# Kernel tuning notes

Measured on AMD Instinct MI355X. Metric: run time of the kernel, lower is better.

Reference implementation:

```python
import jax, jax.numpy as jnp
import numpy as np

D_MODEL = 768
D_STATE = 16
D_CONV = 4
EXPAND = 2
D_INNER = EXPAND * D_MODEL
DT_RANK = (D_MODEL + 15) // 16  # 48
BATCH = 2
SEQ = 1024
LN_EPS = 1e-5


def setup_inputs() -> dict:
    key = jax.random.key(0)
    ks = jax.random.split(key, 12)
    s = 0.02
    inp = {
        "x": jax.random.normal(ks[0], (BATCH, SEQ, D_MODEL), dtype=jnp.float32),
        "in_proj_w": jax.random.normal(ks[1], (2 * D_INNER, D_MODEL), dtype=jnp.float32) * s,
        "conv_w": jax.random.normal(ks[2], (D_INNER, D_CONV), dtype=jnp.float32) * s,
        "conv_b": jnp.zeros((D_INNER,), dtype=jnp.float32),
        "x_proj_w": jax.random.normal(ks[3], (DT_RANK + 2 * D_STATE, D_INNER), dtype=jnp.float32) * s,
        "dt_proj_w": jax.random.normal(ks[4], (D_INNER, DT_RANK), dtype=jnp.float32) * s,
        "dt_proj_b": jnp.full((D_INNER,), -4.0, dtype=jnp.float32),  # softplus(-4) ~ small dt
        "A_log": jnp.log(jnp.broadcast_to(jnp.arange(1, D_STATE + 1, dtype=jnp.float32), (D_INNER, D_STATE))),
        "D": jnp.ones((D_INNER,), dtype=jnp.float32),
        "out_proj_w": jax.random.normal(ks[5], (D_MODEL, D_INNER), dtype=jnp.float32) * s,
        "ln_w": jnp.ones((D_MODEL,), dtype=jnp.float32),
        "ln_b": jnp.zeros((D_MODEL,), dtype=jnp.float32),
    }
    return inp


def _mamba(x, in_proj_w, conv_w, conv_b, x_proj_w, dt_proj_w, dt_proj_b, A_log, D, out_proj_w):
    B, L, _ = x.shape
    # input projection -> [B, L, 2*D_INNER], split into x-branch and gate z
    xz = jnp.einsum("bld,ed->ble", x, in_proj_w)
    xb, z = jnp.split(xz, 2, axis=-1)
    # causal depthwise conv1d along L
    lhs = jnp.transpose(xb, (0, 2, 1))  # [B, D_INNER, L]
    rhs = conv_w[:, None, :]  # [D_INNER, 1, D_CONV]
    xc = jax.lax.conv_general_dilated(
        lhs, rhs, window_strides=(1,), padding=[(D_CONV - 1, 0)],
        dimension_numbers=("NCH", "OIH", "NCH"), feature_group_count=D_INNER)
    xc = jnp.transpose(xc, (0, 2, 1)) + conv_b  # [B, L, D_INNER]
    xc = jax.nn.silu(xc)
    # data-dependent SSM parameters
    x_dbl = jnp.einsum("bld,ed->ble", xc, x_proj_w)  # [B, L, DT_RANK+2*D_STATE]
    dt, Bm, Cm = jnp.split(x_dbl, [DT_RANK, DT_RANK + D_STATE], axis=-1)
    dt = jax.nn.softplus(jnp.einsum("blr,dr->bld", dt, dt_proj_w) + dt_proj_b)  # [B, L, D_INNER]
    A = -jnp.exp(A_log)  # [D_INNER, D_STATE]

    # selective scan over time
    def step(h, inp):
        dt_t, B_t, C_t, u_t = inp  # [B,D_INNER], [B,D_STATE], [B,D_STATE], [B,D_INNER]
        dA = jnp.exp(dt_t[:, :, None] * A)  # [B, D_INNER, D_STATE]
        h = h * dA + (dt_t * u_t)[:, :, None] * B_t[:, None, :]
        y = jnp.einsum("bds,bs->bd", h, C_t)
        return h, y

    h0 = jnp.zeros((B, D_INNER, D_STATE), dtype=x.dtype)
    xs = (jnp.transpose(dt, (1, 0, 2)), jnp.transpose(Bm, (1, 0, 2)),
          jnp.transpose(Cm, (1, 0, 2)), jnp.transpose(xc, (1, 0, 2)))
    _, ys = jax.lax.scan(step, h0, xs)  # ys: [L, B, D_INNER]
    y = jnp.transpose(ys, (1, 0, 2)) + xc * D
    y = y * jax.nn.silu(z)
    return jnp.einsum("ble,de->bld", y, out_proj_w)  # [B, L, D_MODEL]


def reference(x, in_proj_w, conv_w, conv_b, x_proj_w, dt_proj_w, dt_proj_b,
              A_log, D, out_proj_w, ln_w, ln_b):
    residual = x
    h = _mamba(x, in_proj_w, conv_w, conv_b, x_proj_w, dt_proj_w, dt_proj_b, A_log, D, out_proj_w)
    # dropout is identity in eval mode
    y = h + residual
    mu = jnp.mean(y, axis=-1, keepdims=True)
    var = jnp.mean(jnp.square(y - mu), axis=-1, keepdims=True)
    return (y - mu) * jax.lax.rsqrt(var + LN_EPS) * ln_w + ln_b
```

## Files before the change

kernel.cpp:

```cpp
#include <hip/hip_runtime.h>
#include <hip/hip_bf16.h>
#include <math.h>

#define BATCH   2
#define SEQ     1024
#define DMODEL  768
#define DINNER  1536
#define DSTATE  16
#define DTRANK  48
#define NTOK    (BATCH*SEQ)
#define XPROJ_N (DTRANK + 2*DSTATE)
#define XP_PSZ  ((size_t)NTOK * XPROJ_N)

#define LC      32
#define NC      (SEQ/LC)

#define KSPL_IN   2
#define KSPL_OUT  4
#define KSPL_XP   8

typedef unsigned short ushort_t;
typedef __attribute__((ext_vector_type(8))) short bf16x8;
typedef __attribute__((ext_vector_type(4))) float f32x4;

__device__ __forceinline__ ushort_t f2bf(float f) {
    unsigned int u = __float_as_uint(f);
    u += 0x7FFF + ((u >> 16) & 1);
    return (ushort_t)(u >> 16);
}

__global__ __launch_bounds__(256)
void f2b_3(const float* __restrict__ s0, ushort_t* __restrict__ d0, int n0,
           const float* __restrict__ s1, ushort_t* __restrict__ d1, int n1,
           const float* __restrict__ s2, ushort_t* __restrict__ d2, int n2)
{
    const int i = (blockIdx.x * 256 + threadIdx.x) * 4;
    const float* s; ushort_t* d;
    if (i < n0)               { s = s0 + i;            d = d0 + i; }
    else if (i < n0 + n1)     { s = s1 + (i - n0);     d = d1 + (i - n0); }
    else if (i < n0 + n1 + n2){ s = s2 + (i - n0 - n1);d = d2 + (i - n0 - n1); }
    else return;
    const float4 v = *reinterpret_cast<const float4*>(s);
    ushort4 o;
    o.x = f2bf(v.x); o.y = f2bf(v.y); o.z = f2bf(v.z); o.w = f2bf(v.w);
    *reinterpret_cast<ushort4*>(d) = o;
}

#define GLOAD_LDS16(gp, lp) \
    __builtin_amdgcn_global_load_lds((const __attribute__((address_space(1))) void*)(gp), \
                                     (__attribute__((address_space(3))) void*)(lp), 16, 0, 0)

__global__ __launch_bounds__(256)
void gemm_mfma_bt_sk(const ushort_t* __restrict__ A, const ushort_t* __restrict__ W,
                     float* __restrict__ C, int M, int N, int K, int klen)
{
    __shared__ ushort_t As[128 * 32];
    __shared__ ushort_t Bs[128 * 32];

    const int tid  = threadIdx.x;
    const int w    = tid >> 6;
    const int lane = tid & 63;
    const int m0 = blockIdx.y * 128;
    const int n0 = blockIdx.x * 128;
    const int kbeg = blockIdx.z * klen;
    float* Cp = C + (size_t)blockIdx.z * M * N;

    const int lrow = lane >> 2;
    const int lcol = (lane & 3) * 8;

    const ushort_t* ga0 = A + (size_t)(m0 + w * 16 + lrow) * K + kbeg + lcol;
    const ushort_t* ga1 = ga0 + (size_t)64 * K;
    const ushort_t* gb0 = W + (size_t)(n0 + w * 16 + lrow) * K + kbeg + lcol;
    const ushort_t* gb1 = gb0 + (size_t)64 * K;

    ushort_t* lA0 = As + w * 512;
    ushort_t* lA1 = As + 64 * 32 + w * 512;
    ushort_t* lB0 = Bs + w * 512;
    ushort_t* lB1 = Bs + 64 * 32 + w * 512;

    const int wm = w >> 1, wn = w & 1;
    const int fr = lane & 15;
    const int kg = lane >> 4;

    f32x4 acc[4][4] = {};

    for (int kt = 0; kt < klen; kt += 32) {
        __syncthreads();
        GLOAD_LDS16(ga0 + kt, lA0);
        GLOAD_LDS16(ga1 + kt, lA1);
        GLOAD_LDS16(gb0 + kt, lB0);
        GLOAD_LDS16(gb1 + kt, lB1);
        __syncthreads();

        bf16x8 af[4], bfr[4];
        #pragma unroll
        for (int i = 0; i < 4; ++i) {
            af[i]  = *reinterpret_cast<const bf16x8*>(&As[(wm * 64 + i * 16 + fr) * 32 + kg * 8]);
            bfr[i] = *reinterpret_cast<const bf16x8*>(&Bs[(wn * 64 + i * 16 + fr) * 32 + kg * 8]);
        }
        #pragma unroll
        for (int i = 0; i < 4; ++i)
            #pragma unroll
            for (int j = 0; j < 4; ++j)
                acc[i][j] = __builtin_amdgcn_mfma_f32_16x16x32_bf16(af[i], bfr[j], acc[i][j], 0, 0, 0);
    }

    #pragma unroll
    for (int i = 0; i < 4; ++i) {
        const int row_base = m0 + wm * 64 + i * 16 + kg * 4;
        #pragma unroll
        for (int j = 0; j < 4; ++j) {
            const int col = n0 + wn * 64 + j * 16 + fr;
            #pragma unroll
            for (int r = 0; r < 4; ++r)
                Cp[(size_t)(row_base + r) * N + col] = acc[i][j][r];
        }
    }
}

#define BM 64
#define BN 64
#define BK 16

__global__ __launch_bounds__(256)
void gemm_tn_xp(const float* __restrict__ A, const float* __restrict__ W,
                float* __restrict__ C)
{
    __shared__ float As[BK][BM + 4];
    __shared__ float Ws[BK][BN + 4];

    const int M = NTOK, N = XPROJ_N, K = DINNER, lda = DINNER;
    const int kchunk = DINNER / KSPL_XP;

    const int t  = threadIdx.x;
    const int tx = t & 15;
    const int ty = t >> 4;
    const int row0 = blockIdx.y * BM;
    const int col0 = blockIdx.x * BN;
    const int kbeg = blockIdx.z * kchunk;
    const int kend = kbeg + kchunk;
    float* Cp = C + (size_t)blockIdx.z * XP_PSZ;

    const int m_l = t >> 2;
    const int k_l = (t & 3) * 4;

    float acc[4][4] = {};

    for (int kt = kbeg; kt < kend; kt += BK) {
        float4 av, wv;
        {
            const float* ap = A + (size_t)(row0 + m_l) * lda + kt + k_l;
            av = *reinterpret_cast<const float4*>(ap);
        }
        {
            const int wn = col0 + m_l;
            if (wn < N) {
                const float* wp = W + (size_t)wn * K + kt + k_l;
                wv = *reinterpret_cast<const float4*>(wp);
            } else {
                wv = make_float4(0.f, 0.f, 0.f, 0.f);
            }
        }
        __syncthreads();
        As[k_l + 0][m_l] = av.x; As[k_l + 1][m_l] = av.y;
        As[k_l + 2][m_l] = av.z; As[k_l + 3][m_l] = av.w;
        Ws[k_l + 0][m_l] = wv.x; Ws[k_l + 1][m_l] = wv.y;
        Ws[k_l + 2][m_l] = wv.z; Ws[k_l + 3][m_l] = wv.w;
        __syncthreads();

        #pragma unroll
        for (int k = 0; k < BK; ++k) {
            float4 a4 = *reinterpret_cast<const float4*>(&As[k][ty * 4]);
            float4 w4 = *reinterpret_cast<const float4*>(&Ws[k][tx * 4]);
            float af[4] = {a4.x, a4.y, a4.z, a4.w};
            float wf[4] = {w4.x, w4.y, w4.z, w4.w};
            #pragma unroll
            for (int i = 0; i < 4; ++i)
                #pragma unroll
                for (int j = 0; j < 4; ++j)
                    acc[i][j] += af[i] * wf[j];
        }
    }

    #pragma unroll
    for (int i = 0; i < 4; ++i) {
        const int m = row0 + ty * 4 + i;
        #pragma unroll
        for (int j = 0; j < 4; ++j) {
            const int n = col0 + tx * 4 + j;
            if (n < N)
                Cp[(size_t)m * N + n] = acc[i][j];
        }
    }
}

__global__ __launch_bounds__(256)
void gemm_tn_dt(const float* __restrict__ Ap, const float* __restrict__ W,
                const float* __restrict__ bias, float* __restrict__ C)
{
    __shared__ float As[BK][BM + 4];
    __shared__ float Ws[BK][BN + 4];

    const int N = DINNER, K = DTRANK, lda = XPROJ_N;

    const int t  = threadIdx.x;
    const int tx = t & 15;
    const int ty = t >> 4;
    const int row0 = blockIdx.y * BM;
    const int col0 = blockIdx.x * BN;

    const int m_l = t >> 2;
    const int k_l = (t & 3) * 4;

    float acc[4][4] = {};

    for (int kt = 0; kt < K; kt += BK) {
        float4 av = make_float4(0.f, 0.f, 0.f, 0.f);
        {
            const size_t off = (size_t)(row0 + m_l) * lda + kt + k_l;
            #pragma unroll
            for (int p = 0; p < KSPL_XP; ++p) {
                const float4 v = *reinterpret_cast<const float4*>(Ap + p * XP_PSZ + off);
                av.x += v.x; av.y += v.y; av.z += v.z; av.w += v.w;
            }
        }
        float4 wv;
        {
            const int wn = col0 + m_l;
            const float* wp = W + (size_t)wn * K + kt + k_l;
            wv = *reinterpret_cast<const float4*>(wp);
        }
        __syncthreads();
        As[k_l + 0][m_l] = av.x; As[k_l + 1][m_l] = av.y;
        As[k_l + 2][m_l] = av.z; As[k_l + 3][m_l] = av.w;
        Ws[k_l + 0][m_l] = wv.x; Ws[k_l + 1][m_l] = wv.y;
        Ws[k_l + 2][m_l] = wv.z; Ws[k_l + 3][m_l] = wv.w;
        __syncthreads();

        #pragma unroll
        for (int k = 0; k < BK; ++k) {
            float4 a4 = *reinterpret_cast<const float4*>(&As[k][ty * 4]);
            float4 w4 = *reinterpret_cast<const float4*>(&Ws[k][tx * 4]);
            float af[4] = {a4.x, a4.y, a4.z, a4.w};
            float wf[4] = {w4.x, w4.y, w4.z, w4.w};
            #pragma unroll
            for (int i = 0; i < 4; ++i)
                #pragma unroll
                for (int j = 0; j < 4; ++j)
                    acc[i][j] += af[i] * wf[j];
        }
    }

    #pragma unroll
    for (int i = 0; i < 4; ++i) {
        const int m = row0 + ty * 4 + i;
        #pragma unroll
        for (int j = 0; j < 4; ++j) {
            const int n = col0 + tx * 4 + j;
            float v = acc[i][j] + bias[n];
            v = (v > 20.f) ? v : log1pf(expf(v));
            C[(size_t)m * N + n] = v;
        }
    }
}

__global__ __launch_bounds__(256)
void conv_silu(const float* __restrict__ xzA, const float* __restrict__ xzB,
               const float* __restrict__ cw, const float* __restrict__ cb,
               float* __restrict__ xc)
{
    const int vid = blockIdx.x * 256 + threadIdx.x;
    const int c4 = (vid % (DINNER / 4)) * 4;
    const int m  = vid / (DINNER / 4);
    const int l  = m & (SEQ - 1);
    const int R  = 2 * DINNER;

    const float* a = xzA + (size_t)m * R + c4;
    const float* b = xzB + (size_t)m * R + c4;

    float4 W0 = *reinterpret_cast<const float4*>(cw + (c4 + 0) * 4);
    float4 W1 = *reinterpret_cast<const float4*>(cw + (c4 + 1) * 4);
    float4 W2 = *reinterpret_cast<const float4*>(cw + (c4 + 2) * 4);
    float4 W3 = *reinterpret_cast<const float4*>(cw + (c4 + 3) * 4);
    const float4 bias = *reinterpret_cast<const float4*>(cb + c4);

    float4 s0 = *reinterpret_cast<const float4*>(a);
    {
        const float4 t = *reinterpret_cast<const float4*>(b);
        s0.x += t.x; s0.y += t.y; s0.z += t.z; s0.w += t.w;
    }
    float acc0 = bias.x + s0.x * W0.w;
    float acc1 = bias.y + s0.y * W1.w;
    float acc2 = bias.z + s0.z * W2.w;
    float acc3 = bias.w + s0.w * W3.w;

    if (l >= 1) {
        float4 s = *reinterpret_cast<const float4*>(a - R);
        const float4 t = *reinterpret_cast<const float4*>(b - R);
        s.x += t.x; s.y += t.y; s.z += t.z; s.w += t.w;
        acc0 += s.x * W0.z; acc1 += s.y * W1.z; acc2 += s.z * W2.z; acc3 += s.w * W3.z;
    }
    if (l >= 2) {
        float4 s = *reinterpret_cast<const float4*>(a - 2 * R);
        const float4 t = *reinterpret_cast<const float4*>(b - 2 * R);
        s.x += t.x; s.y += t.y; s.z += t.z; s.w += t.w;
        acc0 += s.x * W0.y; acc1 += s.y * W1.y; acc2 += s.z * W2.y; acc3 += s.w * W3.y;
    }
    if (l >= 3) {
        float4 s = *reinterpret_cast<const float4*>(a - 3 * R);
        const float4 t = *reinterpret_cast<const float4*>(b - 3 * R);
        s.x += t.x; s.y += t.y; s.z += t.z; s.w += t.w;
        acc0 += s.x * W0.x; acc1 += s.y * W1.x; acc2 += s.z * W2.x; acc3 += s.w * W3.x;
    }

    float4 o;
    o.x = acc0 / (1.f + __expf(-acc0));
    o.y = acc1 / (1.f + __expf(-acc1));
    o.z = acc2 / (1.f + __expf(-acc2));
    o.w = acc3 / (1.f + __expf(-acc3));
    *reinterpret_cast<float4*>(xc + (size_t)m * DINNER + c4) = o;
}

__global__ __launch_bounds__(256)
void scan_chunk_state(const float* __restrict__ dt, const float* __restrict__ xc,
                      const float* __restrict__ xdblP, const float* __restrict__ A_log,
                      float* __restrict__ hA, float* __restrict__ aP)
{
    __shared__ float B_s[LC * 16];

    const int c  = blockIdx.x;
    const int d0 = blockIdx.y * 256;
    const int b  = blockIdx.z;
    const int t  = threadIdx.x;
    const int d  = d0 + t;

    const size_t row0 = (size_t)b * SEQ + (size_t)c * LC;

    #pragma unroll
    for (int p = 0; p < (LC * 16) / 256; ++p) {
        const int idx = p * 256 + t;
        const int l = idx >> 4, j = idx & 15;
        const size_t off = (row0 + l) * XPROJ_N + DTRANK + j;
        float v = 0.f;
        #pragma unroll
        for (int q = 0; q < KSPL_XP; ++q) v += xdblP[q * XP_PSZ + off];
        B_s[idx] = v;
    }
    __syncthreads();

    float Aval[16];
    #pragma unroll
    for (int q = 0; q < 4; ++q) {
        const float4 a4 = *reinterpret_cast<const float4*>(&A_log[(size_t)d * DSTATE + q * 4]);
        Aval[q*4+0] = -expf(a4.x); Aval[q*4+1] = -expf(a4.y);
        Aval[q*4+2] = -expf(a4.z); Aval[q*4+3] = -expf(a4.w);
    }

    float h[16];
    #pragma unroll
    for (int s = 0; s < 16; ++s) h[s] = 0.f;
    float dts = 0.f;

    #pragma unroll 2
    for (int l = 0; l < LC; ++l) {
        const size_t m = row0 + l;
        const float dtv = dt[m * DINNER + d];
        const float u   = xc[m * DINNER + d];
        const float du  = dtv * u;
        dts += dtv;
        float Bv[16];
        #pragma unroll
        for (int q = 0; q < 4; ++q) {
            const float4 b4 = *reinterpret_cast<const float4*>(&B_s[l * 16 + q * 4]);
            Bv[q*4+0] = b4.x; Bv[q*4+1] = b4.y; Bv[q*4+2] = b4.z; Bv[q*4+3] = b4.w;
        }
        #pragma unroll
        for (int s = 0; s < 16; ++s)
            h[s] = h[s] * __expf(dtv * Aval[s]) + du * Bv[s];
    }

    const size_t o = (((size_t)(b * NC + c) * DINNER) + d) * DSTATE;
    #pragma unroll
    for (int q = 0; q < 4; ++q) {
        float4 hv = make_float4(h[q*4+0], h[q*4+1], h[q*4+2], h[q*4+3]);
        float4 pv = make_float4(__expf(Aval[q*4+0]*dts), __expf(Aval[q*4+1]*dts),
                                __expf(Aval[q*4+2]*dts), __expf(Aval[q*4+3]*dts));
        *reinterpret_cast<float4*>(&hA[o + q*4]) = hv;
        *reinterpret_cast<float4*>(&aP[o + q*4]) = pv;
    }
}

__global__ __launch_bounds__(256)
void scan_combine(float* __restrict__ hA, const float* __restrict__ aP)
{
    const int idx = blockIdx.x * 256 + threadIdx.x;
    const int b  = idx / (DINNER * DSTATE);
    const int ds = idx % (DINNER * DSTATE);
    const size_t stride = (size_t)DINNER * DSTATE;
    const size_t base = (size_t)b * NC * stride + ds;

    float a[NC], p[NC];
    #pragma unroll
    for (int c = 0; c < NC; ++c) {
        a[c] = hA[base + (size_t)c * stride];
        p[c] = aP[base + (size_t)c * stride];
    }
    float h = 0.f;
    #pragma unroll
    for (int c = 0; c < NC; ++c) {
        const float hn = a[c] + h * p[c];
        hA[base + (size_t)c * stride] = h;
        h = hn;
    }
}

__global__ __launch_bounds__(256)
void scan_apply(const float* __restrict__ dt, const float* __restrict__ xc,
                const float* __restrict__ xdblP,
                const float* __restrict__ xzA, const float* __restrict__ xzB,
                const float* __restrict__ A_log, const float* __restrict__ Dp,
                const float* __restrict__ hInit, ushort_t* __restrict__ y)
{
    __shared__ float B_s[LC * 16];
    __shared__ float C_s[LC * 16];

    const int c  = blockIdx.x;
    const int d0 = blockIdx.y * 256;
    const int b  = blockIdx.z;
    const int t  = threadIdx.x;
    const int d  = d0 + t;

    const size_t row0 = (size_t)b * SEQ + (size_t)c * LC;

    #pragma unroll
    for (int p = 0; p < (LC * 16) / 256; ++p) {
        const int idx = p * 256 + t;
        const int l = idx >> 4, j = idx & 15;
        const size_t offB = (row0 + l) * XPROJ_N + DTRANK + j;
        float vb = 0.f, vc = 0.f;
        #pragma unroll
        for (int q = 0; q < KSPL_XP; ++q) {
            vb += xdblP[q * XP_PSZ + offB];
            vc += xdblP[q * XP_PSZ + offB + DSTATE];
        }
        B_s[idx] = vb;
        C_s[idx] = vc;
    }
    __syncthreads();

    float Aval[16];
    #pragma unroll
    for (int q = 0; q < 4; ++q) {
        const float4 a4 = *reinterpret_cast<const float4*>(&A_log[(size_t)d * DSTATE + q * 4]);
        Aval[q*4+0] = -expf(a4.x); Aval[q*4+1] = -expf(a4.y);
        Aval[q*4+2] = -expf(a4.z); Aval[q*4+3] = -expf(a4.w);
    }
    const float Dd = Dp[d];

    const size_t o = (((size_t)(b * NC + c) * DINNER) + d) * DSTATE;
    float h[16];
    #pragma unroll
    for (int q = 0; q < 4; ++q) {
        const float4 h4 = *reinterpret_cast<const float4*>(&hInit[o + q*4]);
        h[q*4+0] = h4.x; h[q*4+1] = h4.y; h[q*4+2] = h4.z; h[q*4+3] = h4.w;
    }

    #pragma unroll 2
    for (int l = 0; l < LC; ++l) {
        const size_t m = row0 + l;
        const float dtv = dt[m * DINNER + d];
        const float u   = xc[m * DINNER + d];
        const size_t zi = m * (2 * DINNER) + DINNER + d;
        const float zv  = xzA[zi] + xzB[zi];
        const float du  = dtv * u;

        float acc = 0.f;
        #pragma unroll
        for (int q = 0; q < 4; ++q) {
            const float4 b4 = *reinterpret_cast<const float4*>(&B_s[l * 16 + q * 4]);
            const float4 c4 = *reinterpret_cast<const float4*>(&C_s[l * 16 + q * 4]);
            const float bb[4] = {b4.x, b4.y, b4.z, b4.w};
            const float cc[4] = {c4.x, c4.y, c4.z, c4.w};
            #pragma unroll
            for (int r = 0; r < 4; ++r) {
                const int s = q * 4 + r;
                h[s] = h[s] * __expf(dtv * Aval[s]) + du * bb[r];
                acc += h[s] * cc[r];
            }
        }

        const float yv  = acc + u * Dd;
        const float sig = 1.f / (1.f + __expf(-zv));
        y[m * DINNER + d] = f2bf(yv * zv * sig);
    }
}

__global__ __launch_bounds__(256)
void ln_kernel(const float* __restrict__ mo, const float* __restrict__ x,
               const float* __restrict__ w, const float* __restrict__ bias,
               float* __restrict__ out)
{
    const int m = blockIdx.x;
    const int t = threadIdx.x;
    const size_t MN = (size_t)NTOK * DMODEL;
    const float* mrow = mo + (size_t)m * DMODEL;
    const float* xrow = x  + (size_t)m * DMODEL;

    float v[3];
    float sum = 0.f, ss = 0.f;
    #pragma unroll
    for (int i = 0; i < 3; ++i) {
        const int col = t + 256 * i;
        float acc = xrow[col];
        #pragma unroll
        for (int p = 0; p < KSPL_OUT; ++p)
            acc += mrow[p * MN + col];
        v[i] = acc;
        sum += acc;
        ss  += acc * acc;
    }
    #pragma unroll
    for (int o = 1; o < 64; o <<= 1) {
        sum += __shfl_xor(sum, o);
        ss  += __shfl_xor(ss, o);
    }
    __shared__ float red[2][4];
    const int wid = t >> 6;
    if ((t & 63) == 0) { red[0][wid] = sum; red[1][wid] = ss; }
    __syncthreads();
    sum = red[0][0] + red[0][1] + red[0][2] + red[0][3];
    ss  = red[1][0] + red[1][1] + red[1][2] + red[1][3];

    const float mu   = sum * (1.f / DMODEL);
    const float var  = ss * (1.f / DMODEL) - mu * mu;
    const float rstd = rsqrtf(var + 1e-5f);

    #pragma unroll
    for (int i = 0; i < 3; ++i) {
        const int col = t + 256 * i;
        out[(size_t)m * DMODEL + col] = (v[i] - mu) * rstd * w[col] + bias[col];
    }
}

extern "C" void kernel_launch(void* const* d_in, const int* in_sizes, int n_in,
                              void* d_out, int out_size, void* d_ws, size_t ws_size,
                              hipStream_t stream)
{
    const float* x          = (const float*)d_in[0];
    const float* in_proj_w  = (const float*)d_in[1];
    const float* conv_w     = (const float*)d_in[2];
    const float* conv_b     = (const float*)d_in[3];
    const float* x_proj_w   = (const float*)d_in[4];
    const float* dt_proj_w  = (const float*)d_in[5];
    const float* dt_proj_b  = (const float*)d_in[6];
    const float* A_log      = (const float*)d_in[7];
    const float* Dp         = (const float*)d_in[8];
    const float* out_proj_w = (const float*)d_in[9];
    const float* ln_w       = (const float*)d_in[10];
    const float* ln_b       = (const float*)d_in[11];
    float* out = (float*)d_out;

    float* ws   = (float*)d_ws;
    float* xz   = ws;
    float* xc   = xz   + (size_t)KSPL_IN * NTOK * 3072;
    float* xdbl = xc   + (size_t)NTOK * 1536;
    float* dt   = xdbl + (size_t)KSPL_XP * XP_PSZ;
    float* mo   = dt   + (size_t)NTOK * 1536;
    ushort_t* xb16 = (ushort_t*)(mo + (size_t)KSPL_OUT * NTOK * 768);
    ushort_t* ipw16 = xb16  + (size_t)NTOK * DMODEL;
    ushort_t* opw16 = ipw16 + (size_t)2 * DINNER * DMODEL;
    ushort_t* ybb   = opw16 + (size_t)DMODEL * DINNER;

    float* xzA = xz;
    float* xzB = xz + (size_t)NTOK * 3072;

    float* aP = mo;
    float* hA = (float*)d_out;

    {
        const int n0 = NTOK * DMODEL;
        const int n1 = 2 * DINNER * DMODEL;
        const int n2 = DMODEL * DINNER;
        const int nvec = (n0 + n1 + n2) / 4;
        f2b_3<<<(nvec + 255) / 256, 256, 0, stream>>>(
            x, xb16, n0, in_proj_w, ipw16, n1, out_proj_w, opw16, n2);
    }

    gemm_mfma_bt_sk<<<dim3(2 * DINNER / 128, NTOK / 128, KSPL_IN), 256, 0, stream>>>(
        xb16, ipw16, xz, NTOK, 2 * DINNER, DMODEL, DMODEL / KSPL_IN);

    conv_silu<<<(NTOK * DINNER / 4) / 256, 256, 0, stream>>>(xzA, xzB, conv_w, conv_b, xc);

    gemm_tn_xp<<<dim3((XPROJ_N + BN - 1) / BN, NTOK / BM, KSPL_XP), 256, 0, stream>>>(
        xc, x_proj_w, xdbl);

    gemm_tn_dt<<<dim3(DINNER / BN, NTOK / BM), 256, 0, stream>>>(
        xdbl, dt_proj_w, dt_proj_b, dt);

    scan_chunk_state<<<dim3(NC, DINNER / 256, BATCH), 256, 0, stream>>>(
        dt, xc, xdbl, A_log, hA, aP);
    scan_combine<<<(BATCH * DINNER * DSTATE) / 256, 256, 0, stream>>>(hA, aP);
    scan_apply<<<dim3(NC, DINNER / 256, BATCH), 256, 0, stream>>>(
        dt, xc, xdbl, xzA, xzB, A_log, Dp, hA, ybb);

    gemm_mfma_bt_sk<<<dim3(DMODEL / 128, NTOK / 128, KSPL_OUT), 256, 0, stream>>>(
        ybb, opw16, mo, NTOK, DMODEL, DINNER, DINNER / KSPL_OUT);

    ln_kernel<<<NTOK, 256, 0, stream>>>(mo, x, ln_w, ln_b, out);
}
```

Baseline: 244.2 us.

## Store GEMM split-K partials and dt in bf16, add workgroup swizzle

The in-proj and out-proj split-K partial outputs and the softplus dt tensor are now written as bf16 instead of fp32, and every consumer (conv_silu, both scan kernels, LayerNorm) converts them back to float on load. This halves the bytes written and read for the largest intermediate tensors, cutting memory traffic across several kernels. The MFMA GEMM also remaps its flat block index in a strided way, likely to spread neighbouring tiles across chiplets or caches. The cost is accuracy: each split-K partial is rounded to bf16 before being summed, which adds error to the output.

```diff
diff --git a/kernel.cpp b/kernel.cpp
--- a/kernel.cpp
+++ b/kernel.cpp
@@ -27,6 +27,9 @@
     unsigned int u = __float_as_uint(f);
     u += 0x7FFF + ((u >> 16) & 1);
     return (ushort_t)(u >> 16);
+}
+__device__ __forceinline__ float bf2f(ushort_t u) {
+    return __uint_as_float((unsigned int)u << 16);
 }
 
 __global__ __launch_bounds__(256)
@@ -52,18 +55,26 @@
 
 __global__ __launch_bounds__(256)
 void gemm_mfma_bt_sk(const ushort_t* __restrict__ A, const ushort_t* __restrict__ W,
-                     float* __restrict__ C, int M, int N, int K, int klen)
+                     ushort_t* __restrict__ C, int M, int N, int K, int klen)
 {
     __shared__ ushort_t As[128 * 32];
     __shared__ ushort_t Bs[128 * 32];
+
+    int flat = blockIdx.x + gridDim.x * (blockIdx.y + gridDim.y * blockIdx.z);
+    const int nwg = gridDim.x * gridDim.y * gridDim.z;
+    flat = (flat & 7) * (nwg >> 3) + (flat >> 3);
+    const int bx = flat % gridDim.x;
+    const int rem = flat / gridDim.x;
+    const int by = rem % gridDim.y;
+    const int bz = rem / gridDim.y;
 
     const int tid  = threadIdx.x;
     const int w    = tid >> 6;
     const int lane = tid & 63;
-    const int m0 = blockIdx.y * 128;
-    const int n0 = blockIdx.x * 128;
-    const int kbeg = blockIdx.z * klen;
-    float* Cp = C + (size_t)blockIdx.z * M * N;
+    const int m0 = by * 128;
+    const int n0 = bx * 128;
+    const int kbeg = bz * klen;
+    ushort_t* Cp = C + (size_t)bz * M * N;
 
     const int lrow = lane >> 2;
     const int lcol = (lane & 3) * 8;
@@ -113,7 +124,7 @@
             const int col = n0 + wn * 64 + j * 16 + fr;
             #pragma unroll
             for (int r = 0; r < 4; ++r)
-                Cp[(size_t)(row_base + r) * N + col] = acc[i][j][r];
+                Cp[(size_t)(row_base + r) * N + col] = f2bf(acc[i][j][r]);
         }
     }
 }
@@ -129,7 +140,7 @@
     __shared__ float As[BK][BM + 4];
     __shared__ float Ws[BK][BN + 4];
 
-    const int M = NTOK, N = XPROJ_N, K = DINNER, lda = DINNER;
+    const int N = XPROJ_N, K = DINNER, lda = DINNER;
     const int kchunk = DINNER / KSPL_XP;
 
     const int t  = threadIdx.x;
@@ -196,7 +207,7 @@
 
 __global__ __launch_bounds__(256)
 void gemm_tn_dt(const float* __restrict__ Ap, const float* __restrict__ W,
-                const float* __restrict__ bias, float* __restrict__ C)
+                const float* __restrict__ bias, ushort_t* __restrict__ C)
 {
     __shared__ float As[BK][BM + 4];
     __shared__ float Ws[BK][BN + 4];
@@ -259,13 +270,13 @@
             const int n = col0 + tx * 4 + j;
             float v = acc[i][j] + bias[n];
             v = (v > 20.f) ? v : log1pf(expf(v));
-            C[(size_t)m * N + n] = v;
-        }
-    }
-}
-
-__global__ __launch_bounds__(256)
-void conv_silu(const float* __restrict__ xzA, const float* __restrict__ xzB,
+            C[(size_t)m * N + n] = f2bf(v);
+        }
+    }
+}
+
+__global__ __launch_bounds__(256)
+void conv_silu(const ushort_t* __restrict__ xzA, const ushort_t* __restrict__ xzB,
                const float* __restrict__ cw, const float* __restrict__ cb,
                float* __restrict__ xc)
 {
@@ -275,8 +286,8 @@
     const int l  = m & (SEQ - 1);
     const int R  = 2 * DINNER;
 
-    const float* a = xzA + (size_t)m * R + c4;
-    const float* b = xzB + (size_t)m * R + c4;
+    const ushort_t* a = xzA + (size_t)m * R + c4;
+    const ushort_t* b = xzB + (size_t)m * R + c4;
 
     float4 W0 = *reinterpret_cast<const float4*>(cw + (c4 + 0) * 4);
     float4 W1 = *reinterpret_cast<const float4*>(cw + (c4 + 1) * 4);
@@ -284,33 +295,39 @@
     float4 W3 = *reinterpret_cast<const float4*>(cw + (c4 + 3) * 4);
     const float4 bias = *reinterpret_cast<const float4*>(cb + c4);
 
-    float4 s0 = *reinterpret_cast<const float4*>(a);
+    float acc0 = bias.x, acc1 = bias.y, acc2 = bias.z, acc3 = bias.w;
+
     {
-        const float4 t = *reinterpret_cast<const float4*>(b);
-        s0.x += t.x; s0.y += t.y; s0.z += t.z; s0.w += t.w;
-    }
-    float acc0 = bias.x + s0.x * W0.w;
-    float acc1 = bias.y + s0.y * W1.w;
-    float acc2 = bias.z + s0.z * W2.w;
-    float acc3 = bias.w + s0.w * W3.w;
-
+        const ushort4 ua = *reinterpret_cast<const ushort4*>(a);
+        const ushort4 ub = *reinterpret_cast<const ushort4*>(b);
+        acc0 += (bf2f(ua.x) + bf2f(ub.x)) * W0.w;
+        acc1 += (bf2f(ua.y) + bf2f(ub.y)) * W1.w;
+        acc2 += (bf2f(ua.z) + bf2f(ub.z)) * W2.w;
+        acc3 += (bf2f(ua.w) + bf2f(ub.w)) * W3.w;
+    }
     if (l >= 1) {
-        float4 s = *reinterpret_cast<const float4*>(a - R);
-        const float4 t = *reinterpret_cast<const float4*>(b - R);
-        s.x += t.x; s.y += t.y; s.z += t.z; s.w += t.w;
-        acc0 += s.x * W0.z; acc1 += s.y * W1.z; acc2 += s.z * W2.z; acc3 += s.w * W3.z;
+        const ushort4 ua = *reinterpret_cast<const ushort4*>(a - R);
+        const ushort4 ub = *reinterpret_cast<const ushort4*>(b - R);
+        acc0 += (bf2f(ua.x) + bf2f(ub.x)) * W0.z;
+        acc1 += (bf2f(ua.y) + bf2f(ub.y)) * W1.z;
+        acc2 += (bf2f(ua.z) + bf2f(ub.z)) * W2.z;
+        acc3 += (bf2f(ua.w) + bf2f(ub.w)) * W3.z;
     }
     if (l >= 2) {
-        float4 s = *reinterpret_cast<const float4*>(a - 2 * R);
-        const float4 t = *reinterpret_cast<const float4*>(b - 2 * R);
-        s.x += t.x; s.y += t.y; s.z += t.z; s.w += t.w;
-        acc0 += s.x * W0.y; acc1 += s.y * W1.y; acc2 += s.z * W2.y; acc3 += s.w * W3.y;
+        const ushort4 ua = *reinterpret_cast<const ushort4*>(a - 2 * R);
+        const ushort4 ub = *reinterpret_cast<const ushort4*>(b - 2 * R);
+        acc0 += (bf2f(ua.x) + bf2f(ub.x)) * W0.y;
+        acc1 += (bf2f(ua.y) + bf2f(ub.y)) * W1.y;
+        acc2 += (bf2f(ua.z) + bf2f(ub.z)) * W2.y;
+        acc3 += (bf2f(ua.w) + bf2f(ub.w)) * W3.y;
     }
     if (l >= 3) {
-        float4 s = *reinterpret_cast<const float4*>(a - 3 * R);
-        const float4 t = *reinterpret_cast<const float4*>(b - 3 * R);
-        s.x += t.x; s.y += t.y; s.z += t.z; s.w += t.w;
-        acc0 += s.x * W0.x; acc1 += s.y * W1.x; acc2 += s.z * W2.x; acc3 += s.w * W3.x;
+        const ushort4 ua = *reinterpret_cast<const ushort4*>(a - 3 * R);
+        const ushort4 ub = *reinterpret_cast<const ushort4*>(b - 3 * R);
+        acc0 += (bf2f(ua.x) + bf2f(ub.x)) * W0.x;
+        acc1 += (bf2f(ua.y) + bf2f(ub.y)) * W1.x;
+        acc2 += (bf2f(ua.z) + bf2f(ub.z)) * W2.x;
+        acc3 += (bf2f(ua.w) + bf2f(ub.w)) * W3.x;
     }
 
     float4 o;
@@ -322,7 +339,7 @@
 }
 
 __global__ __launch_bounds__(256)
-void scan_chunk_state(const float* __restrict__ dt, const float* __restrict__ xc,
+void scan_chunk_state(const ushort_t* __restrict__ dt, const float* __restrict__ xc,
                       const float* __restrict__ xdblP, const float* __restrict__ A_log,
                       float* __restrict__ hA, float* __restrict__ aP)
 {
@@ -364,7 +381,7 @@
     #pragma unroll 2
     for (int l = 0; l < LC; ++l) {
         const size_t m = row0 + l;
-        const float dtv = dt[m * DINNER + d];
+        const float dtv = bf2f(dt[m * DINNER + d]);
         const float u   = xc[m * DINNER + d];
         const float du  = dtv * u;
         dts += dtv;
@@ -415,9 +432,9 @@
 }
 
 __global__ __launch_bounds__(256)
-void scan_apply(const float* __restrict__ dt, const float* __restrict__ xc,
+void scan_apply(const ushort_t* __restrict__ dt, const float* __restrict__ xc,
                 const float* __restrict__ xdblP,
-                const float* __restrict__ xzA, const float* __restrict__ xzB,
+                const ushort_t* __restrict__ xzA, const ushort_t* __restrict__ xzB,
                 const float* __restrict__ A_log, const float* __restrict__ Dp,
                 const float* __restrict__ hInit, ushort_t* __restrict__ y)
 {
@@ -468,10 +485,10 @@
     #pragma unroll 2
     for (int l = 0; l < LC; ++l) {
         const size_t m = row0 + l;
-        const float dtv = dt[m * DINNER + d];
+        const float dtv = bf2f(dt[m * DINNER + d]);
         const float u   = xc[m * DINNER + d];
         const size_t zi = m * (2 * DINNER) + DINNER + d;
-        const float zv  = xzA[zi] + xzB[zi];
+        const float zv  = bf2f(xzA[zi]) + bf2f(xzB[zi]);
         const float du  = dtv * u;
 
         float acc = 0.f;
@@ -496,15 +513,15 @@
 }
 
 __global__ __launch_bounds__(256)
-void ln_kernel(const float* __restrict__ mo, const float* __restrict__ x,
+void ln_kernel(const ushort_t* __restrict__ mo, const float* __restrict__ x,
                const float* __restrict__ w, const float* __restrict__ bias,
                float* __restrict__ out)
 {
     const int m = blockIdx.x;
     const int t = threadIdx.x;
     const size_t MN = (size_t)NTOK * DMODEL;
-    const float* mrow = mo + (size_t)m * DMODEL;
-    const float* xrow = x  + (size_t)m * DMODEL;
+    const ushort_t* mrow = mo + (size_t)m * DMODEL;
+    const float* xrow = x + (size_t)m * DMODEL;
 
     float v[3];
     float sum = 0.f, ss = 0.f;
@@ -514,7 +531,7 @@
         float acc = xrow[col];
         #pragma unroll
         for (int p = 0; p < KSPL_OUT; ++p)
-            acc += mrow[p * MN + col];
+            acc += bf2f(mrow[p * MN + col]);
         v[i] = acc;
         sum += acc;
         ss  += acc * acc;
@@ -561,20 +578,20 @@
     float* out = (float*)d_out;
 
     float* ws   = (float*)d_ws;
-    float* xz   = ws;
-    float* xc   = xz   + (size_t)KSPL_IN * NTOK * 3072;
-    float* xdbl = xc   + (size_t)NTOK * 1536;
-    float* dt   = xdbl + (size_t)KSPL_XP * XP_PSZ;
-    float* mo   = dt   + (size_t)NTOK * 1536;
-    ushort_t* xb16 = (ushort_t*)(mo + (size_t)KSPL_OUT * NTOK * 768);
+    float* xc   = ws;
+    float* xdbl = xc + (size_t)NTOK * 1536;
+    ushort_t* xz   = (ushort_t*)(xdbl + (size_t)KSPL_XP * XP_PSZ);
+    ushort_t* dt   = xz + (size_t)KSPL_IN * NTOK * 3072;
+    ushort_t* mo   = dt + (size_t)NTOK * 1536;
+    ushort_t* xb16 = mo + (size_t)KSPL_OUT * NTOK * 768;
     ushort_t* ipw16 = xb16  + (size_t)NTOK * DMODEL;
     ushort_t* opw16 = ipw16 + (size_t)2 * DINNER * DMODEL;
     ushort_t* ybb   = opw16 + (size_t)DMODEL * DINNER;
 
-    float* xzA = xz;
-    float* xzB = xz + (size_t)NTOK * 3072;
-
-    float* aP = mo;
+    ushort_t* xzA = xz;
+    ushort_t* xzB = xz + (size_t)NTOK * 3072;
+
+    float* aP = (float*)mo;
     float* hA = (float*)d_out;
 
     {
```

After: 237.0 us. 1.03x faster.
